# Kernel tuning notes

Measured on AMD Instinct MI355X. Metric: run time of the kernel, lower is better.

Reference implementation:

```python
import jax, jax.numpy as jnp
import numpy as np

# ---- static geometry derived from truncation (matches torch __init__) ----
T = 127
N_LAT_NH = T + 1                                   # 128 NH latitudes
LONS = [20 + 4 * i for i in range(N_LAT_NH)]       # octahedral reduced grid
CUMS = np.concatenate([[0], np.cumsum(np.array(LONS + LONS[::-1]))]).astype(int)
HZW_NH = np.minimum(4 + np.arange(N_LAT_NH), T)    # cubic truncation: m_max = nlon//4 - 1, capped at T
N_LATS_PER_M = np.array([(HZW_NH >= m).sum() for m in range(T + 1)])
L_SYM_FULL = (T + 3) // 2                          # 65 rows before dropping row 0
L_ANT = (T + 2) // 2                               # 64
N_VARS = 128
BATCH, ENS = 4, 1


def _tri_masks():
    """Zero-padded triangular structure of the per-m Legendre matrices."""
    sym = np.zeros((T + 1, L_SYM_FULL, N_LAT_NH), np.float32)
    ant = np.zeros((T + 1, L_ANT, N_LAT_NH), np.float32)
    for m in range(T + 1):
        n_lats = int(N_LATS_PER_M[m])
        ms = (T - m + 3) // 2
        off = L_SYM_FULL - ms
        sym[m, off:, N_LAT_NH - n_lats:] = 1.0
        if (m + 1) % 2 == 1:
            sym[m, off, :] = 0.0
        ma = (T - m + 2) // 2
        off = L_ANT - ma
        ant[m, off:, N_LAT_NH - n_lats:] = 1.0
        if m % 2 == 1:
            ant[m, off, :] = 0.0
    return sym[:, 1:, :], ant   # module drops first symmetric row -> [128,64,128]


def setup_inputs() -> dict:
    key = jax.random.key(0)
    k1, k2, k3 = jax.random.split(key, 3)
    n_grid = int(CUMS[-1])
    x = jax.random.normal(k1, (BATCH, ENS, n_grid, N_VARS), jnp.float32)
    sm, am = _tri_masks()
    # random stand-ins for (gaussian-weight-fused) Legendre polynomials, with the exact
    # triangular zero structure the module builds from ecTrans assets
    symmetric = jax.random.normal(k2, sm.shape, jnp.float32) * jnp.asarray(sm)
    antisymmetric = jax.random.normal(k3, am.shape, jnp.float32) * jnp.asarray(am)
    return {"x": x, "symmetric": symmetric, "antisymmetric": antisymmetric}


def reference(x, symmetric, antisymmetric):
    """Octahedral SHT forward: ragged longitudinal rfft -> hemispheric fold -> per-m Legendre matmuls.

    Returns spectrum [b, e, l, m, vars, 2] (real/imag stacked on last axis).
    """
    n_lat = 2 * N_LAT_NH
    north, south = [], []
    # loop is over structurally distinct (ragged) latitude ring lengths; NH lat i and its
    # SH mirror (lat n_lat-1-i) share nlon/truncation, so batch them in one FFT call.
    for i in range(N_LAT_NH):
        j = n_lat - 1 - i
        nlon = LONS[i]
        xn = x[:, :, CUMS[i]:CUMS[i + 1], :]           # [b,e,nlon,v]
        xs = x[:, :, CUMS[j]:CUMS[j + 1], :]
        xp = jnp.stack([xn, xs], axis=2)               # [b,e,2,nlon,v]
        f = jnp.fft.rfft(xp, axis=3) / nlon            # torch norm='forward'
        m_hi = int(HZW_NH[i]) + 1                      # keep m <= highest zonal wavenumber
        f = f[:, :, :, :m_hi, :]
        f = jnp.pad(f, ((0, 0), (0, 0), (0, 0), (0, T + 1 - m_hi), (0, 0)))
        north.append(f[:, :, 0])
        south.append(f[:, :, 1])                       # index i <-> lat n_lat-1-i: already pole-mirrored
    north = jnp.stack(north, axis=2)                   # [b,e,n_lat_nh,m,v] complex64
    south = jnp.stack(south, axis=2)
    # hemispheric symmetry of Legendre polynomials
    sym = north + south
    anti = north - south
    # per-m truncated Legendre contractions over NH latitudes (n)
    out_s = jnp.einsum('mln,benmv->belmv', symmetric, sym)     # [b,e,64,m,v]
    out_a = jnp.einsum('mln,benmv->belmv', antisymmetric, anti)
    # interleave symmetric (l-m even) and antisymmetric (l-m odd) rows -> full l axis (128)
    spec = jnp.stack([out_s, out_a], axis=3)
    b, e, L, _, M, V = spec.shape
    spec = spec.reshape(b, e, 2 * L, M, V)             # [b,e,l,m,v] complex, lower triangle zeros
    return jnp.stack([spec.real, spec.imag], axis=-1)  # real view [b,e,l,m,v,2]
```

## Files before the change

### kernel.cpp

```cpp
#include <hip/hip_runtime.h>
#include <hip/hip_bf16.h>

#define NGRID 70144
#define NV 128

typedef float f32x4 __attribute__((ext_vector_type(4)));
typedef short short8 __attribute__((ext_vector_type(8)));

__device__ __forceinline__ float4 f4add(float4 a, float4 b){ return make_float4(a.x+b.x, a.y+b.y, a.z+b.z, a.w+b.w); }
__device__ __forceinline__ float4 f4sub(float4 a, float4 b){ return make_float4(a.x-b.x, a.y-b.y, a.z-b.z, a.w-b.w); }

__device__ __forceinline__ unsigned f2bf(float f){
  return (unsigned)__bfloat16_as_ushort(__float2bfloat16(f));
}
__device__ __forceinline__ float bf2f(unsigned h){ return __uint_as_float(h<<16); }
__device__ __forceinline__ unsigned packsplit(float f){
  unsigned h = f2bf(f);
  unsigned l = f2bf(f - bf2f(h));
  return (h<<16) | l;
}
__device__ __forceinline__ int swzc(int c){ return (c ^ (c>>3)) & 7; }

__device__ __forceinline__ void unpack_frag(int4 a, int4 b, short8 &bh, short8 &bl){
  int h0 = (int)(((unsigned)a.x >> 16) | ((unsigned)a.y & 0xFFFF0000u));
  int h1 = (int)(((unsigned)a.z >> 16) | ((unsigned)a.w & 0xFFFF0000u));
  int h2 = (int)(((unsigned)b.x >> 16) | ((unsigned)b.y & 0xFFFF0000u));
  int h3 = (int)(((unsigned)b.z >> 16) | ((unsigned)b.w & 0xFFFF0000u));
  int l0 = (int)(((unsigned)a.x & 0xFFFFu) | ((unsigned)a.y << 16));
  int l1 = (int)(((unsigned)a.z & 0xFFFFu) | ((unsigned)a.w << 16));
  int l2 = (int)(((unsigned)b.x & 0xFFFFu) | ((unsigned)b.y << 16));
  int l3 = (int)(((unsigned)b.z & 0xFFFFu) | ((unsigned)b.w << 16));
  int4 H = make_int4(h0,h1,h2,h3), L = make_int4(l0,l1,l2,l3);
  bh = *(short8*)&H; bl = *(short8*)&L;
}

__global__ void fill_tw(unsigned short* __restrict__ twA){
  int ring = blockIdx.x, t = blockIdx.y;
  int N = 20+4*ring, H = N/2, JC = H+1;
  int mhi = (5+ring<128)?(5+ring):128;
  int Mpad = ((mhi+15)>>4)<<4;
  int Kpad = ((JC+31)>>5)<<5;
  long off = 0;
  for(int r=0;r<ring;r++){
    int mh=(5+r<128)?(5+r):128, jc=11+2*r;
    off += 4L*(((mh+15)>>4)<<4)*(((jc+31)>>5)<<5);
  }
  long MK = (long)Mpad*Kpad;
  unsigned short* hiT = twA + off + (long)(t*2)*MK;
  unsigned short* loT = hiT + MK;
  float invN = 1.0f/(float)N;
  for(long idx = threadIdx.x; idx < MK; idx += 256){
    int m = (int)(idx / Kpad), j = (int)(idx % Kpad);
    float val = 0.f;
    if(m < mhi && j < JC){
      int p = (m*j) % N;
      float th = 6.2831853071795864f * (float)p * invN;
      float sn, cs; __sincosf(th,&sn,&cs);
      val = (t ? -sn : cs) * invN;
    }
    unsigned h = f2bf(val);
    unsigned l = f2bf(val - bf2f(h));
    hiT[idx] = (unsigned short)h;
    loT[idx] = (unsigned short)l;
  }
}

__global__ __launch_bounds__(256) void dft_mfma(const float* __restrict__ x,
                                                const unsigned short* __restrict__ twA,
                                                unsigned* __restrict__ Gp){
  int bx = blockIdx.x;
  int ring = 127 - (bx >> 1);
  int type = bx & 1;
  int b = blockIdx.y;
  int N = 20+4*ring, H = N/2, JC = H+1;
  int mhi = (5+ring<128)?(5+ring):128;
  int Mt_n = (mhi+15)>>4;
  int KT = (JC+31)>>5;
  int Kpad = KT<<5;
  int Mpad = Mt_n<<4;

  long off = 0;
  for(int r=0;r<ring;r++){
    int mh=(5+r<128)?(5+r):128, jc=11+2*r;
    off += 4L*(((mh+15)>>4)<<4)*(((jc+31)>>5)<<5);
  }
  long MK = (long)Mpad*Kpad;
  const unsigned short* Ahi = twA + off + (long)(type*2)*MK;
  const unsigned short* Alo = Ahi + MK;

  const float* xn = x + ((long)b*NGRID + (long)ring*(2*ring+18))*NV;
  long a1 = ring+1;
  const float* xs = x + ((long)b*NGRID + (NGRID - a1*(2*a1+18)))*NV;

  __shared__ __align__(16) unsigned Bp[8192];

  int tid = threadIdx.x;
  int jb = tid >> 5, vp = tid & 31;
  int wave = tid >> 6, lane = tid & 63;
  int jj = lane & 15, kb = lane >> 4;

  f32x4 acc[8][4];
  #pragma unroll
  for(int Mt=0;Mt<8;Mt++)
    #pragma unroll
    for(int ct=0;ct<4;ct++) acc[Mt][ct] = (f32x4){0.f,0.f,0.f,0.f};

  for(int kt=0; kt<KT; ++kt){
    __syncthreads();
    float4 fS[4], fA[4];
    #pragma unroll
    for(int dj=0;dj<4;dj++){
      int j = kt*32 + jb*4 + dj;
      float4 z = make_float4(0.f,0.f,0.f,0.f);
      float4 nj=z, sj=z, np=z, sp=z;
      if(j < JC){
        nj = *(const float4*)&xn[(long)j*NV + vp*4];
        sj = *(const float4*)&xs[(long)j*NV + vp*4];
        if(j > 0 && j < H){
          int jp = N - j;
          np = *(const float4*)&xn[(long)jp*NV + vp*4];
          sp = *(const float4*)&xs[(long)jp*NV + vp*4];
        }
      }
      float4 e  = f4add(nj, sj), o  = f4sub(nj, sj);
      float4 ep = f4add(np, sp), op = f4sub(np, sp);
      fS[dj] = type ? f4sub(e, ep) : f4add(e, ep);
      fA[dj] = type ? f4sub(o, op) : f4add(o, op);
    }
    #pragma unroll
    for(int dv=0;dv<4;dv++){
      int c0 = (vp*4+dv)*2;
      int4 wS = make_int4((int)packsplit(((const float*)&fS[0])[dv]),
                          (int)packsplit(((const float*)&fS[1])[dv]),
                          (int)packsplit(((const float*)&fS[2])[dv]),
                          (int)packsplit(((const float*)&fS[3])[dv]));
      *(int4*)&Bp[c0*32 + ((jb*4) ^ (swzc(c0)<<2))] = wS;
      int c1 = c0 + 1;
      int4 wA = make_int4((int)packsplit(((const float*)&fA[0])[dv]),
                          (int)packsplit(((const float*)&fA[1])[dv]),
                          (int)packsplit(((const float*)&fA[2])[dv]),
                          (int)packsplit(((const float*)&fA[3])[dv]));
      *(int4*)&Bp[c1*32 + ((jb*4) ^ (swzc(c1)<<2))] = wA;
    }
    __syncthreads();
    short8 bh[4], bl[4];
    #pragma unroll
    for(int ct=0;ct<4;ct++){
      int c = wave*64 + ct*16 + jj;
      int sw = swzc(c)<<2;
      int4 pa = *(const int4*)&Bp[c*32 + ((kb*8) ^ sw)];
      int4 pb = *(const int4*)&Bp[c*32 + ((kb*8+4) ^ sw)];
      unpack_frag(pa, pb, bh[ct], bl[ct]);
    }
    #pragma unroll
    for(int Mt=0;Mt<8;Mt++){
      if(Mt < Mt_n){
        long ao = (long)(Mt*16 + jj)*Kpad + kt*32 + kb*8;
        short8 ah = *(const short8*)&Ahi[ao];
        short8 al = *(const short8*)&Alo[ao];
        #pragma unroll
        for(int ct=0;ct<4;ct++){
          acc[Mt][ct] = __builtin_amdgcn_mfma_f32_16x16x32_bf16(ah, bh[ct], acc[Mt][ct], 0,0,0);
          acc[Mt][ct] = __builtin_amdgcn_mfma_f32_16x16x32_bf16(al, bh[ct], acc[Mt][ct], 0,0,0);
          acc[Mt][ct] = __builtin_amdgcn_mfma_f32_16x16x32_bf16(ah, bl[ct], acc[Mt][ct], 0,0,0);
        }
      }
    }
  }
  #pragma unroll
  for(int Mt=0;Mt<8;Mt++){
    if(Mt < Mt_n){
      #pragma unroll
      for(int ct=0;ct<4;ct++){
        int c = wave*64 + ct*16 + jj;
        int s = c & 1, v = c >> 1;
        #pragma unroll
        for(int reg=0;reg<4;reg++){
          int m = Mt*16 + (kb<<2) + reg;
          if(m < mhi){
            Gp[(long)((s*2+type)*128 + m)*65536 + (long)ring*512 + b*128 + v]
              = packsplit(acc[Mt][ct][reg]);
          }
        }
      }
    }
  }
}

__global__ void w_split(const float* __restrict__ Wsym, const float* __restrict__ Want,
                        unsigned short* __restrict__ Wh, unsigned short* __restrict__ Wl){
  long i = (long)blockIdx.x*256 + threadIdx.x;
  const float* W = (i < 1048576) ? Wsym : Want;
  float w = W[i & 1048575];
  unsigned h = f2bf(w);
  unsigned l = f2bf(w - bf2f(h));
  Wh[i] = (unsigned short)h;
  Wl[i] = (unsigned short)l;
}

__global__ __launch_bounds__(256) void legendre_mfma(const unsigned short* __restrict__ Wh,
                                                     const unsigned short* __restrict__ Wl,
                                                     const unsigned* __restrict__ Gp,
                                                     float* __restrict__ out){
  int m = blockIdx.x, b = blockIdx.y, s = blockIdx.z;
  __shared__ __align__(16) unsigned Bp[8192];
  int tid = threadIdx.x;
  int wave = tid >> 6, lane = tid & 63;
  int jj = lane & 15, kb = lane >> 4;

  int kt0 = (m > 4) ? ((m-4) >> 5) : 0;

  const unsigned short* WA = Wh + (long)(s*128+m)*8192;
  const unsigned short* WB = Wl + (long)(s*128+m)*8192;
  int ri = tid & 1, v = tid >> 1;
  long gC0 = (long)((s*2+ri)*128 + m)*65536 + (long)b*128 + v;

  f32x4 acc[4][4];
  #pragma unroll
  for(int a=0;a<4;a++)
    #pragma unroll
    for(int q=0;q<4;q++) acc[a][q] = (f32x4){0.f,0.f,0.f,0.f};

  int swT = swzc(tid)<<2;
  for(int kt=kt0; kt<4; ++kt){
    __syncthreads();
    #pragma unroll
    for(int k4=0;k4<32;k4+=4){
      int4 w = make_int4((int)Gp[gC0 + (long)(kt*32+k4+0)*512],
                         (int)Gp[gC0 + (long)(kt*32+k4+1)*512],
                         (int)Gp[gC0 + (long)(kt*32+k4+2)*512],
                         (int)Gp[gC0 + (long)(kt*32+k4+3)*512]);
      *(int4*)&Bp[tid*32 + (k4 ^ swT)] = w;
    }
    __syncthreads();
    short8 bh[4], bl[4];
    #pragma unroll
    for(int nt=0;nt<4;nt++){
      int c = (wave*4+nt)*16 + jj;
      int sw = swzc(c)<<2;
      int4 pa = *(const int4*)&Bp[c*32 + ((kb*8) ^ sw)];
      int4 pb = *(const int4*)&Bp[c*32 + ((kb*8+4) ^ sw)];
      unpack_frag(pa, pb, bh[nt], bl[nt]);
    }
    #pragma unroll
    for(int Mt=0;Mt<4;Mt++){
      long ao = (long)(Mt*16 + jj)*128 + kt*32 + kb*8;
      short8 ah = *(const short8*)&WA[ao];
      short8 al = *(const short8*)&WB[ao];
      #pragma unroll
      for(int nt=0;nt<4;nt++){
        acc[Mt][nt] = __builtin_amdgcn_mfma_f32_16x16x32_bf16(ah, bh[nt], acc[Mt][nt], 0,0,0);
        acc[Mt][nt] = __builtin_amdgcn_mfma_f32_16x16x32_bf16(al, bh[nt], acc[Mt][nt], 0,0,0);
        acc[Mt][nt] = __builtin_amdgcn_mfma_f32_16x16x32_bf16(ah, bl[nt], acc[Mt][nt], 0,0,0);
      }
    }
  }
  int r4 = (lane>>4)<<2;
  #pragma unroll
  for(int Mt=0;Mt<4;Mt++){
    #pragma unroll
    for(int nt=0;nt<4;nt++){
      int c = (wave*4+nt)*16 + jj;
      #pragma unroll
      for(int reg=0;reg<4;reg++){
        int l = Mt*16 + r4 + reg;
        out[((long)(b*128 + 2*l + s)*128 + m)*256 + c] = acc[Mt][nt][reg];
      }
    }
  }
}

extern "C" void kernel_launch(void* const* d_in, const int* in_sizes, int n_in,
                              void* d_out, int out_size, void* d_ws, size_t ws_size,
                              hipStream_t stream) {
  const float* x    = (const float*)d_in[0];
  const float* Wsym = (const float*)d_in[1];
  const float* Want = (const float*)d_in[2];
  float* out = (float*)d_out;

  long TWA = 0;
  for(int r=0;r<128;r++){
    int mh=(5+r<128)?(5+r):128, jc=11+2*r;
    TWA += 4L*(((mh+15)/16)*16)*(((jc+31)/32)*32);
  }
  size_t gpOffB = (size_t)TWA*2;
  if(gpOffB < 8388608) gpOffB = 8388608;
  gpOffB = (gpOffB + 255) & ~(size_t)255;

  unsigned short* twA = (unsigned short*)d_ws;
  unsigned* Gp = (unsigned*)((char*)d_ws + gpOffB);
  unsigned short* Wh = (unsigned short*)d_ws;
  unsigned short* Wl = Wh + 2097152;

  hipLaunchKernelGGL(fill_tw,       dim3(128,2),   dim3(256), 0, stream, twA);
  hipLaunchKernelGGL(dft_mfma,      dim3(256,4),   dim3(256), 0, stream, x, twA, Gp);
  hipLaunchKernelGGL(w_split,       dim3(8192),    dim3(256), 0, stream, Wsym, Want, Wh, Wl);
  hipLaunchKernelGGL(legendre_mfma, dim3(128,4,2), dim3(256), 0, stream, Wh, Wl, Gp, out);
}
```

Measured before the change: 415.3 us.

## Split DFT blocks over m-tile chunks and precompute twiddle offsets at compile time

```diff
diff --git a/kernel.cpp b/kernel.cpp
--- a/kernel.cpp
+++ b/kernel.cpp
@@ -34,58 +34,95 @@
   bh = *(short8*)&H; bl = *(short8*)&L;
 }
 
+struct TileT { unsigned char ring, type, mc; };
+constexpr int calc_ntiles(){
+  int n=0;
+  for(int r=0;r<128;r++){
+    int mhi=(5+r<128)?(5+r):128;
+    int mtn=(mhi+15)/16;
+    n += 2*((mtn+3)/4);
+  }
+  return n;
+}
+constexpr int NTILES = calc_ntiles();
+struct Tiles { TileT t[NTILES]; };
+constexpr Tiles make_tiles(){
+  Tiles T{}; int k=0;
+  for(int r=127;r>=0;r--){
+    int mhi=(5+r<128)?(5+r):128;
+    int mtn=(mhi+15)/16;
+    int nc=(mtn+3)/4;
+    for(int mc=0;mc<nc;mc++)
+      for(int tp=0;tp<2;tp++){
+        T.t[k].ring=(unsigned char)r; T.t[k].type=(unsigned char)tp; T.t[k].mc=(unsigned char)mc; k++;
+      }
+  }
+  return T;
+}
+__constant__ Tiles TILES = make_tiles();
+
+struct Offs { long o[129]; };
+constexpr Offs make_offs(){
+  Offs O{}; long off=0;
+  for(int r=0;r<128;r++){
+    O.o[r]=off;
+    int mh=(5+r<128)?(5+r):128, jc=11+2*r;
+    off += 4L*(((mh+15)/16)*16)*(((jc+31)/32)*32);
+  }
+  O.o[128]=off;
+  return O;
+}
+__constant__ Offs TWOFF = make_offs();
+constexpr long TWATOT = make_offs().o[128];
+
 __global__ void fill_tw(unsigned short* __restrict__ twA){
   int ring = blockIdx.x, t = blockIdx.y;
   int N = 20+4*ring, H = N/2, JC = H+1;
   int mhi = (5+ring<128)?(5+ring):128;
   int Mpad = ((mhi+15)>>4)<<4;
   int Kpad = ((JC+31)>>5)<<5;
-  long off = 0;
-  for(int r=0;r<ring;r++){
-    int mh=(5+r<128)?(5+r):128, jc=11+2*r;
-    off += 4L*(((mh+15)>>4)<<4)*(((jc+31)>>5)<<5);
-  }
   long MK = (long)Mpad*Kpad;
-  unsigned short* hiT = twA + off + (long)(t*2)*MK;
+  unsigned short* hiT = twA + TWOFF.o[ring] + (long)(t*2)*MK;
   unsigned short* loT = hiT + MK;
   float invN = 1.0f/(float)N;
-  for(long idx = threadIdx.x; idx < MK; idx += 256){
-    int m = (int)(idx / Kpad), j = (int)(idx % Kpad);
-    float val = 0.f;
-    if(m < mhi && j < JC){
-      int p = (m*j) % N;
-      float th = 6.2831853071795864f * (float)p * invN;
-      float sn, cs; __sincosf(th,&sn,&cs);
-      val = (t ? -sn : cs) * invN;
-    }
-    unsigned h = f2bf(val);
-    unsigned l = f2bf(val - bf2f(h));
-    hiT[idx] = (unsigned short)h;
-    loT[idx] = (unsigned short)l;
-  }
-}
-
-__global__ __launch_bounds__(256) void dft_mfma(const float* __restrict__ x,
-                                                const unsigned short* __restrict__ twA,
-                                                unsigned* __restrict__ Gp){
-  int bx = blockIdx.x;
-  int ring = 127 - (bx >> 1);
-  int type = bx & 1;
+  int tid = threadIdx.x;
+  for(int m=0;m<Mpad;m++){
+    int p0   = (int)(((long)m*tid) % N);
+    int step = (int)(((long)m*256) % N);
+    int p = p0;
+    for(int j=tid;j<Kpad;j+=256){
+      float val = 0.f;
+      if(m < mhi && j < JC){
+        float th = 6.2831853071795864f * (float)p * invN;
+        float sn, cs; __sincosf(th,&sn,&cs);
+        val = (t ? -sn : cs) * invN;
+      }
+      unsigned h = f2bf(val);
+      unsigned l = f2bf(val - bf2f(h));
+      long idx = (long)m*Kpad + j;
+      hiT[idx] = (unsigned short)h;
+      loT[idx] = (unsigned short)l;
+      p += step; if(p>=N) p-=N;
+    }
+  }
+}
+
+__global__ __launch_bounds__(256,3) void dft_mfma(const float* __restrict__ x,
+                                                  const unsigned short* __restrict__ twA,
+                                                  unsigned* __restrict__ Gp){
+  TileT tl = TILES.t[blockIdx.x];
+  int ring = tl.ring, type = tl.type;
   int b = blockIdx.y;
   int N = 20+4*ring, H = N/2, JC = H+1;
   int mhi = (5+ring<128)?(5+ring):128;
-  int Mt_n = (mhi+15)>>4;
+  int MtN = (mhi+15)>>4;
+  int Mt0 = tl.mc*4;
   int KT = (JC+31)>>5;
   int Kpad = KT<<5;
-  int Mpad = Mt_n<<4;
-
-  long off = 0;
-  for(int r=0;r<ring;r++){
-    int mh=(5+r<128)?(5+r):128, jc=11+2*r;
-    off += 4L*(((mh+15)>>4)<<4)*(((jc+31)>>5)<<5);
-  }
+  int Mpad = MtN<<4;
+
   long MK = (long)Mpad*Kpad;
-  const unsigned short* Ahi = twA + off + (long)(type*2)*MK;
+  const unsigned short* Ahi = twA + TWOFF.o[ring] + (long)(type*2)*MK;
   const unsigned short* Alo = Ahi + MK;
 
   const float* xn = x + ((long)b*NGRID + (long)ring*(2*ring+18))*NV;
@@ -99,9 +136,9 @@
   int wave = tid >> 6, lane = tid & 63;
   int jj = lane & 15, kb = lane >> 4;
 
-  f32x4 acc[8][4];
+  f32x4 acc[4][4];
   #pragma unroll
-  for(int Mt=0;Mt<8;Mt++)
+  for(int Mt=0;Mt<4;Mt++)
     #pragma unroll
     for(int ct=0;ct<4;ct++) acc[Mt][ct] = (f32x4){0.f,0.f,0.f,0.f};
 
@@ -153,9 +190,9 @@
       unpack_frag(pa, pb, bh[ct], bl[ct]);
     }
     #pragma unroll
-    for(int Mt=0;Mt<8;Mt++){
-      if(Mt < Mt_n){
-        long ao = (long)(Mt*16 + jj)*Kpad + kt*32 + kb*8;
+    for(int Mt=0;Mt<4;Mt++){
+      if(Mt0+Mt < MtN){
+        long ao = (long)((Mt0+Mt)*16 + jj)*Kpad + kt*32 + kb*8;
         short8 ah = *(const short8*)&Ahi[ao];
         short8 al = *(const short8*)&Alo[ao];
         #pragma unroll
@@ -168,15 +205,15 @@
     }
   }
   #pragma unroll
-  for(int Mt=0;Mt<8;Mt++){
-    if(Mt < Mt_n){
+  for(int Mt=0;Mt<4;Mt++){
+    if(Mt0+Mt < MtN){
       #pragma unroll
       for(int ct=0;ct<4;ct++){
         int c = wave*64 + ct*16 + jj;
         int s = c & 1, v = c >> 1;
         #pragma unroll
         for(int reg=0;reg<4;reg++){
-          int m = Mt*16 + (kb<<2) + reg;
+          int m = (Mt0+Mt)*16 + (kb<<2) + reg;
           if(m < mhi){
             Gp[(long)((s*2+type)*128 + m)*65536 + (long)ring*512 + b*128 + v]
               = packsplit(acc[Mt][ct][reg]);
@@ -278,12 +315,7 @@
   const float* Want = (const float*)d_in[2];
   float* out = (float*)d_out;
 
-  long TWA = 0;
-  for(int r=0;r<128;r++){
-    int mh=(5+r<128)?(5+r):128, jc=11+2*r;
-    TWA += 4L*(((mh+15)/16)*16)*(((jc+31)/32)*32);
-  }
-  size_t gpOffB = (size_t)TWA*2;
+  size_t gpOffB = (size_t)TWATOT*2;
   if(gpOffB < 8388608) gpOffB = 8388608;
   gpOffB = (gpOffB + 255) & ~(size_t)255;
 
@@ -292,8 +324,8 @@
   unsigned short* Wh = (unsigned short*)d_ws;
   unsigned short* Wl = Wh + 2097152;
 
-  hipLaunchKernelGGL(fill_tw,       dim3(128,2),   dim3(256), 0, stream, twA);
-  hipLaunchKernelGGL(dft_mfma,      dim3(256,4),   dim3(256), 0, stream, x, twA, Gp);
-  hipLaunchKernelGGL(w_split,       dim3(8192),    dim3(256), 0, stream, Wsym, Want, Wh, Wl);
-  hipLaunchKernelGGL(legendre_mfma, dim3(128,4,2), dim3(256), 0, stream, Wh, Wl, Gp, out);
-}
+  hipLaunchKernelGGL(fill_tw,       dim3(128,2),     dim3(256), 0, stream, twA);
+  hipLaunchKernelGGL(dft_mfma,      dim3(NTILES,4),  dim3(256), 0, stream, x, twA, Gp);
+  hipLaunchKernelGGL(w_split,       dim3(8192),      dim3(256), 0, stream, Wsym, Want, Wh, Wl);
+  hipLaunchKernelGGL(legendre_mfma, dim3(128,4,2),   dim3(256), 0, stream, Wh, Wl, Gp, out);
+}
```

After: 386.5 us. 6.9% less time.
